# Performance work log

Measured on AMD Instinct MI355X. Metric: run time of the kernel, lower is better.

## Reference

```python
import jax, jax.numpy as jnp
import numpy as np

EMBED = 1024  # embed_dim = hidden_dim = out_dim (n_head=1)
NQ, NK = 4096, 4096
NEG = 1e16


def setup_inputs() -> dict:
    key = jax.random.key(0)
    ks = jax.random.split(key, 10)
    stdv = 1.0 / np.sqrt(EMBED)
    lin = lambda kk: jax.random.uniform(kk, (EMBED, EMBED), jnp.float32, -stdv, stdv)
    vec = lambda kk: jax.random.uniform(kk, (EMBED,), jnp.float32, -stdv, stdv)
    return {
        "q": jax.random.normal(ks[0], (NQ, EMBED), jnp.float32),
        "k": jax.random.normal(ks[1], (NK, EMBED), jnp.float32),
        "mask": jax.random.randint(ks[2], (NQ, NK), 0, 2, jnp.int32),
        "wei": jax.random.uniform(ks[3], (NQ, NK), jnp.float32),
        "Wq": lin(ks[4]), "bq": vec(ks[5]),
        "Wk": lin(ks[6]), "bk": vec(ks[7]),
        "Wp": lin(ks[8]), "bp": vec(ks[9]),
    }


def reference(q, k, mask, wei, Wq, bq, Wk, bk, Wp, bp):
    # Linear projections (torch Linear: x @ W.T + b)
    kx = k @ Wk.T + bk                      # [NK, D]
    qx = q @ Wq.T + bq                      # [NQ, D]
    # dot_product score
    score = qx @ kx.T                       # [NQ, NK]
    bias = (mask.astype(jnp.int32) - 1).astype(score.dtype) * NEG
    score = jax.nn.softmax(score + bias, axis=-1)
    # second weighted+masked softmax pass
    score = jax.nn.softmax(score * wei + bias, axis=-1)
    out = (score @ kx) @ Wp.T + bp          # [NQ, D]
    return out, score
```

## Files before the change

### kernel.cpp

```cpp
#include <hip/hip_runtime.h>


typedef __bf16 bf16;
typedef __bf16 bf16x8 __attribute__((ext_vector_type(8)));
typedef __bf16 bf16x4 __attribute__((ext_vector_type(4)));
typedef float  f32x4  __attribute__((ext_vector_type(4)));
typedef float  f32x16 __attribute__((ext_vector_type(16)));
typedef int    i32x4  __attribute__((ext_vector_type(4)));

typedef __attribute__((address_space(1))) void as1_void;
typedef __attribute__((address_space(3))) void as3_void;

#define NQ  4096
#define NKK 4096
#define EMB 1024

#define BM 128
#define BN 128
#define BK 32

__device__ __forceinline__ void gld_lds16(const void* g, void* l) {
    __builtin_amdgcn_global_load_lds((as1_void*)g, (as3_void*)l, 16, 0, 0);
}

__global__ __launch_bounds__(256) void prep_all(
    const float* __restrict__ q, const float* __restrict__ k,
    const float* __restrict__ Wq, const float* __restrict__ Wk, const float* __restrict__ Wp,
    bf16* __restrict__ qh, bf16* __restrict__ ql,
    bf16* __restrict__ kh, bf16* __restrict__ kl,
    bf16* __restrict__ Wqh, bf16* __restrict__ Wql,
    bf16* __restrict__ Wkh, bf16* __restrict__ Wkl,
    bf16* __restrict__ Wph, bf16* __restrict__ Wpl,
    int nqk, int nw)
{
    const int z = blockIdx.y;
    const float* s; bf16* h; bf16* l; int n;
    switch (z) {
        case 0:  s = q;  h = qh;  l = ql;  n = nqk; break;
        case 1:  s = k;  h = kh;  l = kl;  n = nqk; break;
        case 2:  s = Wq; h = Wqh; l = Wql; n = nw;  break;
        case 3:  s = Wk; h = Wkh; l = Wkl; n = nw;  break;
        default: s = Wp; h = Wph; l = Wpl; n = nw;  break;
    }
    const int i = (blockIdx.x * 256 + threadIdx.x) * 4;
    if (i >= n) return;
    f32x4 v = *(const f32x4*)(s + i);
    bf16x4 hv, lv;
#pragma unroll
    for (int c = 0; c < 4; c++) {
        float x = v[c];
        bf16 hh = (bf16)x;
        hv[c] = hh;
        lv[c] = (bf16)(x - (float)hh);
    }
    *(bf16x4*)(h + i) = hv;
    *(bf16x4*)(l + i) = lv;
}

template<int NS, int MODE>
__global__ __launch_bounds__(256) void reduce_k(
    const float* __restrict__ P, const float* __restrict__ bias,
    float* __restrict__ of, bf16* __restrict__ oh, int n, int Nld)
{
    const int i = (blockIdx.x * 256 + threadIdx.x) * 4;
    if (i >= n) return;
    f32x4 v = *(const f32x4*)(P + i);
#pragma unroll
    for (int s = 1; s < NS; s++)
        v += *(const f32x4*)(P + (size_t)s * n + i);
    if (MODE == 1)
        v += *(const f32x4*)(bias + (i & (Nld - 1)));
    if (MODE == 0) {
        bf16x4 o;
#pragma unroll
        for (int c = 0; c < 4; c++) o[c] = (bf16)v[c];
        *(bf16x4*)(oh + i) = o;
    } else {
        *(f32x4*)(of + i) = v;
    }
}

template<int NSPLIT, int HAS_BIAS, int OUT_BF16>
__global__ __launch_bounds__(256) void gemm_bt(
    const bf16* __restrict__ A, const bf16* __restrict__ B,
    const float* __restrict__ bias,
    float* __restrict__ Cf, bf16* __restrict__ Cb,
    int M, int N, int Ksub, int lda, int ldb)
{
    __shared__ bf16 sA[BM * BK];
    __shared__ bf16 sB[BN * BK];
    const int t    = threadIdx.x;
    const int wave = t >> 6;
    const int lane = t & 63;
    const int l31  = lane & 31;
    const int lhi  = lane >> 5;
    const int wm   = wave >> 1;
    const int wn   = wave & 1;
    const int bm   = blockIdx.y * BM;
    const int bn   = blockIdx.x * BN;
    const int srow = t >> 2;
    const int gseg = (t & 3) ^ ((srow >> 1) & 3);
    const int rsw  = (l31 >> 1) & 3;
    const int kz   = (NSPLIT > 0) ? (int)blockIdx.z : 0;

    A += (size_t)kz * Ksub;
    B += (size_t)kz * Ksub;
    if (NSPLIT > 0) Cf += (size_t)kz * M * N;

    const bf16* ga = A + (size_t)(bm + srow) * lda + gseg * 8;
    const bf16* gb = B + (size_t)(bn + srow) * ldb + gseg * 8;
    char* lA = (char*)sA + wave * 1024;
    char* lB = (char*)sB + wave * 1024;

    f32x16 acc[2][2] = {};

    for (int k0 = 0; k0 < Ksub; k0 += BK) {
        __syncthreads();
        gld_lds16(ga + k0,                      lA);
        gld_lds16(ga + (size_t)64 * lda + k0,   lA + 4096);
        gld_lds16(gb + k0,                      lB);
        gld_lds16(gb + (size_t)64 * ldb + k0,   lB + 4096);
        __syncthreads();
        bf16x8 af[2][2], bfr[2][2];
#pragma unroll
        for (int mi = 0; mi < 2; mi++)
#pragma unroll
            for (int kh = 0; kh < 2; kh++)
                af[mi][kh] = *(const bf16x8*)
                    &sA[(wm * 64 + mi * 32 + l31) * BK + ((kh * 2 + lhi) ^ rsw) * 8];
#pragma unroll
        for (int nj = 0; nj < 2; nj++)
#pragma unroll
            for (int kh = 0; kh < 2; kh++)
                bfr[nj][kh] = *(const bf16x8*)
                    &sB[(wn * 64 + nj * 32 + l31) * BK + ((kh * 2 + lhi) ^ rsw) * 8];
#pragma unroll
        for (int kh = 0; kh < 2; kh++)
#pragma unroll
            for (int mi = 0; mi < 2; mi++)
#pragma unroll
                for (int nj = 0; nj < 2; nj++)
                    acc[mi][nj] = __builtin_amdgcn_mfma_f32_32x32x16_bf16(
                        af[mi][kh], bfr[nj][kh], acc[mi][nj], 0, 0, 0);
    }

#pragma unroll
    for (int mi = 0; mi < 2; mi++)
#pragma unroll
        for (int nj = 0; nj < 2; nj++) {
            const int cg = bn + wn * 64 + nj * 32 + l31;
            const float bv = HAS_BIAS ? bias[cg] : 0.0f;
#pragma unroll
            for (int r = 0; r < 16; r++) {
                const int rg = bm + wm * 64 + mi * 32 + (r & 3) + 8 * (r >> 2) + 4 * lhi;
                const float v = acc[mi][nj][r] + bv;
                const size_t idx = (size_t)rg * N + cg;
                if (NSPLIT > 0)    Cf[idx] = v;
                else if (OUT_BF16) Cb[idx] = (bf16)v;
                else               Cf[idx] = v;
            }
        }
}

template<int BATCH, int HAS_BIAS, int HILO>
__global__ __launch_bounds__(256) void gemm_bt_split(
    const bf16* __restrict__ Ah0, const bf16* __restrict__ Al0,
    const bf16* __restrict__ Bh0, const bf16* __restrict__ Bl0,
    const float* __restrict__ bias0, bf16* __restrict__ Ch0, bf16* __restrict__ Cl0,
    const bf16* __restrict__ Ah1, const bf16* __restrict__ Al1,
    const bf16* __restrict__ Bh1, const bf16* __restrict__ Bl1,
    const float* __restrict__ bias1, bf16* __restrict__ Ch1, bf16* __restrict__ Cl1,
    float* __restrict__ Cf,
    int M, int N, int K)
{
    __shared__ bf16 sAh[BM * BK], sAl[BM * BK], sBh[BN * BK], sBl[BN * BK];
    const int t    = threadIdx.x;
    const int wave = t >> 6;
    const int lane = t & 63;
    const int l31  = lane & 31;
    const int lhi  = lane >> 5;
    const int wm   = wave >> 1;
    const int wn   = wave & 1;
    const int bm   = blockIdx.y * BM;
    const int bn   = blockIdx.x * BN;
    const int srow = t >> 2;
    const int gseg = (t & 3) ^ ((srow >> 1) & 3);
    const int rsw  = (l31 >> 1) & 3;

    const int mt = BATCH ? (int)blockIdx.z : 0;

    const bf16* Ah = (BATCH && mt) ? Ah1 : Ah0;
    const bf16* Al = (BATCH && mt) ? Al1 : Al0;
    const bf16* Bh = (BATCH && mt) ? Bh1 : Bh0;
    const bf16* Bl = (BATCH && mt) ? Bl1 : Bl0;
    const float* bias = (BATCH && mt) ? bias1 : bias0;
    bf16* Ch = (BATCH && mt) ? Ch1 : Ch0;
    bf16* Cl = (BATCH && mt) ? Cl1 : Cl0;

    const size_t offA = (size_t)(bm + srow) * K + gseg * 8;
    const size_t offB = (size_t)(bn + srow) * K + gseg * 8;
    char* lAh = (char*)sAh + wave * 1024;
    char* lAl = (char*)sAl + wave * 1024;
    char* lBh = (char*)sBh + wave * 1024;
    char* lBl = (char*)sBl + wave * 1024;

    f32x16 acc[2][2] = {};

    for (int k0 = 0; k0 < K; k0 += BK) {
        __syncthreads();
        gld_lds16(Ah + offA + k0,                  lAh);
        gld_lds16(Ah + offA + (size_t)64 * K + k0, lAh + 4096);
        gld_lds16(Al + offA + k0,                  lAl);
        gld_lds16(Al + offA + (size_t)64 * K + k0, lAl + 4096);
        gld_lds16(Bh + offB + k0,                  lBh);
        gld_lds16(Bh + offB + (size_t)64 * K + k0, lBh + 4096);
        gld_lds16(Bl + offB + k0,                  lBl);
        gld_lds16(Bl + offB + (size_t)64 * K + k0, lBl + 4096);
        __syncthreads();
#pragma unroll
        for (int kh = 0; kh < 2; kh++) {
            const int ksw = ((kh * 2 + lhi) ^ rsw) * 8;
            bf16x8 ah[2], al[2], bh2[2], bl2[2];
#pragma unroll
            for (int mi = 0; mi < 2; mi++) {
                const int ro = (wm * 64 + mi * 32 + l31) * BK + ksw;
                ah[mi] = *(const bf16x8*)&sAh[ro];
                al[mi] = *(const bf16x8*)&sAl[ro];
            }
#pragma unroll
            for (int nj = 0; nj < 2; nj++) {
                const int ro = (wn * 64 + nj * 32 + l31) * BK + ksw;
                bh2[nj] = *(const bf16x8*)&sBh[ro];
                bl2[nj] = *(const bf16x8*)&sBl[ro];
            }
#pragma unroll
            for (int mi = 0; mi < 2; mi++)
#pragma unroll
                for (int nj = 0; nj < 2; nj++) {
                    acc[mi][nj] = __builtin_amdgcn_mfma_f32_32x32x16_bf16(al[mi], bh2[nj], acc[mi][nj], 0, 0, 0);
                    acc[mi][nj] = __builtin_amdgcn_mfma_f32_32x32x16_bf16(ah[mi], bl2[nj], acc[mi][nj], 0, 0, 0);
                    acc[mi][nj] = __builtin_amdgcn_mfma_f32_32x32x16_bf16(ah[mi], bh2[nj], acc[mi][nj], 0, 0, 0);
                }
        }
    }

#pragma unroll
    for (int mi = 0; mi < 2; mi++)
#pragma unroll
        for (int nj = 0; nj < 2; nj++) {
            const int cg = bn + wn * 64 + nj * 32 + l31;
            const float bv = HAS_BIAS ? bias[cg] : 0.0f;
#pragma unroll
            for (int r = 0; r < 16; r++) {
                const int rg = bm + wm * 64 + mi * 32 + (r & 3) + 8 * (r >> 2) + 4 * lhi;
                const float v = acc[mi][nj][r] + bv;
                const size_t idx = (size_t)rg * N + cg;
                if (HILO) {
                    const bf16 hh = (bf16)v;
                    Ch[idx] = hh;
                    Cl[idx] = (bf16)(v - (float)hh);
                } else {
                    Cf[idx] = v;
                }
            }
        }
}

__global__ __launch_bounds__(256, 2) void gemm_score_kxp(
    const bf16* __restrict__ Ah, const bf16* __restrict__ Al,
    const bf16* __restrict__ Bh, const bf16* __restrict__ Bl,
    float* __restrict__ Cf,
    const bf16* __restrict__ Wp, const bf16* __restrict__ Kx,
    bf16* __restrict__ kxpT)
{
    __shared__ bf16 smem[24576];
    const int t    = threadIdx.x;
    const int wave = t >> 6;
    const int lane = t & 63;
    const int l31  = lane & 31;
    const int lhi  = lane >> 5;
    const int srow = t >> 2;
    const int gseg = (t & 3) ^ ((srow >> 1) & 3);
    const int rsw  = (l31 >> 1) & 3;
    const int bid  = blockIdx.x;

    if (bid < 512) {
        bf16* sAh = smem;
        bf16* sAl = smem + 4096;
        bf16* sBh = smem + 8192;
        bf16* sBl = smem + 16384;
        const int bm = (bid >> 4) * 128;
        const int bn = (bid & 15) * 256;
        const int K  = EMB, N = NKK;

        const size_t offA = (size_t)(bm + srow) * K + gseg * 8;
        const size_t offB = (size_t)(bn + srow) * K + gseg * 8;
        char* lAh = (char*)sAh + wave * 1024;
        char* lAl = (char*)sAl + wave * 1024;
        char* lBh = (char*)sBh + wave * 1024;
        char* lBl = (char*)sBl + wave * 1024;

        f32x16 acc[4][2] = {};

        for (int k0 = 0; k0 < K; k0 += BK) {
            __syncthreads();
            gld_lds16(Ah + offA + k0,                  lAh);
            gld_lds16(Ah + offA + (size_t)64 * K + k0, lAh + 4096);
            gld_lds16(Al + offA + k0,                  lAl);
            gld_lds16(Al + offA + (size_t)64 * K + k0, lAl + 4096);
#pragma unroll
            for (int rb = 0; rb < 4; rb++) {
                gld_lds16(Bh + offB + (size_t)(64 * rb) * K + k0, lBh + rb * 4096);
                gld_lds16(Bl + offB + (size_t)(64 * rb) * K + k0, lBl + rb * 4096);
            }
            __syncthreads();
#pragma unroll
            for (int kh = 0; kh < 2; kh++) {
                const int ksw = ((kh * 2 + lhi) ^ rsw) * 8;
                bf16x8 a_h[4], a_l[4], b_h[2], b_l[2];
#pragma unroll
                for (int mi = 0; mi < 4; mi++) {
                    const int ro = (mi * 32 + l31) * BK + ksw;
                    a_h[mi] = *(const bf16x8*)&sAh[ro];
                    a_l[mi] = *(const bf16x8*)&sAl[ro];
                }
#pragma unroll
                for (int nj = 0; nj < 2; nj++) {
                    const int ro = (wave * 64 + nj * 32 + l31) * BK + ksw;
                    b_h[nj] = *(const bf16x8*)&sBh[ro];
                    b_l[nj] = *(const bf16x8*)&sBl[ro];
                }
#pragma unroll
                for (int mi = 0; mi < 4; mi++)
#pragma unroll
                    for (int nj = 0; nj < 2; nj++) {
                        acc[mi][nj] = __builtin_amdgcn_mfma_f32_32x32x16_bf16(a_l[mi], b_h[nj], acc[mi][nj], 0, 0, 0);
                        acc[mi][nj] = __builtin_amdgcn_mfma_f32_32x32x16_bf16(a_h[mi], b_l[nj], acc[mi][nj], 0, 0, 0);
                        acc[mi][nj] = __builtin_amdgcn_mfma_f32_32x32x16_bf16(a_h[mi], b_h[nj], acc[mi][nj], 0, 0, 0);
                    }
            }
        }

#pragma unroll
        for (int mi = 0; mi < 4; mi++)
#pragma unroll
            for (int nj = 0; nj < 2; nj++) {
                const int cg = bn + wave * 64 + nj * 32 + l31;
#pragma unroll
                for (int r = 0; r < 16; r++) {
                    const int rg = bm + mi * 32 + (r & 3) + 8 * (r >> 2) + 4 * lhi;
                    Cf[(size_t)rg * N + cg] = acc[mi][nj][r];
                }
            }
    } else {
        bf16* sA = smem;
        bf16* sB = smem + 4096;
        const int id = bid - 512;
        const int bn = (id & 31) * 128;
        const int bm = (id >> 5) * 128;
        const int K  = EMB, N = NKK;
        const int wm = wave >> 1;
        const int wn = wave & 1;

        const bf16* ga = Wp + (size_t)(bm + srow) * K + gseg * 8;
        const bf16* gb = Kx + (size_t)(bn + srow) * K + gseg * 8;
        char* lA = (char*)sA + wave * 1024;
        char* lB = (char*)sB + wave * 1024;

        f32x16 acc[2][2] = {};

        for (int k0 = 0; k0 < K; k0 += BK) {
            __syncthreads();
            gld_lds16(ga + k0,                    lA);
            gld_lds16(ga + (size_t)64 * K + k0,   lA + 4096);
            gld_lds16(gb + k0,                    lB);
            gld_lds16(gb + (size_t)64 * K + k0,   lB + 4096);
            __syncthreads();
            bf16x8 af[2][2], bfr[2][2];
#pragma unroll
            for (int mi = 0; mi < 2; mi++)
#pragma unroll
                for (int kh = 0; kh < 2; kh++)
                    af[mi][kh] = *(const bf16x8*)
                        &sA[(wm * 64 + mi * 32 + l31) * BK + ((kh * 2 + lhi) ^ rsw) * 8];
#pragma unroll
            for (int nj = 0; nj < 2; nj++)
#pragma unroll
                for (int kh = 0; kh < 2; kh++)
                    bfr[nj][kh] = *(const bf16x8*)
                        &sB[(wn * 64 + nj * 32 + l31) * BK + ((kh * 2 + lhi) ^ rsw) * 8];
#pragma unroll
            for (int kh = 0; kh < 2; kh++)
#pragma unroll
                for (int mi = 0; mi < 2; mi++)
#pragma unroll
                    for (int nj = 0; nj < 2; nj++)
                        acc[mi][nj] = __builtin_amdgcn_mfma_f32_32x32x16_bf16(
                            af[mi][kh], bfr[nj][kh], acc[mi][nj], 0, 0, 0);
        }

#pragma unroll
        for (int mi = 0; mi < 2; mi++)
#pragma unroll
            for (int nj = 0; nj < 2; nj++) {
                const int cg = bn + wn * 64 + nj * 32 + l31;
#pragma unroll
                for (int r = 0; r < 16; r++) {
                    const int rg = bm + wm * 64 + mi * 32 + (r & 3) + 8 * (r >> 2) + 4 * lhi;
                    kxpT[(size_t)rg * N + cg] = (bf16)acc[mi][nj][r];
                }
            }
    }
}

__device__ __forceinline__ float wred_max(float v) {
#pragma unroll
    for (int off = 32; off > 0; off >>= 1) v = fmaxf(v, __shfl_xor(v, off));
    return v;
}
__device__ __forceinline__ float wred_sum(float v) {
#pragma unroll
    for (int off = 32; off > 0; off >>= 1) v += __shfl_xor(v, off);
    return v;
}

__global__ __launch_bounds__(256) void softmax2_kernel(
    float* __restrict__ score, const int* __restrict__ mask,
    const float* __restrict__ wei, bf16* __restrict__ scoreb)
{
    __shared__ float sred[4];
    const int row = blockIdx.x;
    const int t   = threadIdx.x;
    const size_t base = (size_t)row * NKK + (size_t)t * 16;
    const int wv = t >> 6, ln = t & 63;

    float l[16], w[16];
    unsigned mb = 0;
#pragma unroll
    for (int c = 0; c < 4; c++) {
        *(f32x4*)(l + 4 * c) = *(const f32x4*)(score + base + 4 * c);
        *(f32x4*)(w + 4 * c) = *(const f32x4*)(wei + base + 4 * c);
        i32x4 mv = *(const i32x4*)(mask + base + 4 * c);
#pragma unroll
        for (int j = 0; j < 4; j++) if (mv[j] != 0) mb |= 1u << (4 * c + j);
    }

    float mx = -__builtin_inff();
#pragma unroll
    for (int s = 0; s < 16; s++) if (mb & (1u << s)) mx = fmaxf(mx, l[s]);
    mx = wred_max(mx);
    if (ln == 0) sred[wv] = mx;
    __syncthreads();
    mx = fmaxf(fmaxf(sred[0], sred[1]), fmaxf(sred[2], sred[3]));
    __syncthreads();
    float sum = 0.f;
#pragma unroll
    for (int s = 0; s < 16; s++) {
        const float e = (mb & (1u << s)) ? __expf(l[s] - mx) : 0.f;
        l[s] = e; sum += e;
    }
    sum = wred_sum(sum);
    if (ln == 0) sred[wv] = sum;
    __syncthreads();
    sum = sred[0] + sred[1] + sred[2] + sred[3];
    __syncthreads();
    const float inv1 = 1.0f / sum;

#pragma unroll
    for (int s = 0; s < 16; s++) l[s] = l[s] * inv1 * w[s];

    float mx2 = -__builtin_inff();
#pragma unroll
    for (int s = 0; s < 16; s++) if (mb & (1u << s)) mx2 = fmaxf(mx2, l[s]);
    mx2 = wred_max(mx2);
    if (ln == 0) sred[wv] = mx2;
    __syncthreads();
    mx2 = fmaxf(fmaxf(sred[0], sred[1]), fmaxf(sred[2], sred[3]));
    __syncthreads();
    float sum2 = 0.f;
#pragma unroll
    for (int s = 0; s < 16; s++) {
        const float e = (mb & (1u << s)) ? __expf(l[s] - mx2) : 0.f;
        l[s] = e; sum2 += e;
    }
    sum2 = wred_sum(sum2);
    if (ln == 0) sred[wv] = sum2;
    __syncthreads();
    sum2 = sred[0] + sred[1] + sred[2] + sred[3];
    const float inv2 = 1.0f / sum2;

#pragma unroll
    for (int c = 0; c < 4; c++) {
        f32x4 pv;
#pragma unroll
        for (int j = 0; j < 4; j++) pv[j] = l[4 * c + j] * inv2;
        __builtin_nontemporal_store(pv, (f32x4*)(score + base + 4 * c));
#pragma unroll
        for (int j = 0; j < 4; j++) l[4 * c + j] = pv[j];
    }
    bf16x8 b0, b1;
#pragma unroll
    for (int j = 0; j < 8; j++) { b0[j] = (bf16)l[j]; b1[j] = (bf16)l[8 + j]; }
    *(bf16x8*)(scoreb + base)     = b0;
    *(bf16x8*)(scoreb + base + 8) = b1;
}

extern "C" void kernel_launch(void* const* d_in, const int* in_sizes, int n_in,
                              void* d_out, int out_size, void* d_ws, size_t ws_size,
                              hipStream_t stream)
{
    (void)in_sizes; (void)n_in; (void)out_size;
    const float* q    = (const float*)d_in[0];
    const float* k    = (const float*)d_in[1];
    const int*   mask = (const int*)  d_in[2];
    const float* wei  = (const float*)d_in[3];
    const float* Wq   = (const float*)d_in[4];
    const float* bq   = (const float*)d_in[5];
    const float* Wk   = (const float*)d_in[6];
    const float* bk   = (const float*)d_in[7];
    const float* Wp   = (const float*)d_in[8];
    const float* bp   = (const float*)d_in[9];

    float* out   = (float*)d_out;
    float* score = (float*)d_out + (size_t)NQ * EMB;

    char* ws = (char*)d_ws;
    size_t off = 0;
    auto alloc = [&](size_t bytes) -> char* {
        char* p = ws + off; off += (bytes + 255) & ~(size_t)255; return p;
    };
    const size_t n_qk = (size_t)NQ * EMB;
    const size_t n_w  = (size_t)EMB * EMB;
    const size_t n_sc = (size_t)NQ * NKK;

    bf16* qh   = (bf16*)alloc(n_qk * 2);
    bf16* ql   = (bf16*)alloc(n_qk * 2);
    bf16* kh   = (bf16*)alloc(n_qk * 2);
    bf16* kl   = (bf16*)alloc(n_qk * 2);
    bf16* qxh  = (bf16*)alloc(n_qk * 2);
    bf16* qxl  = (bf16*)alloc(n_qk * 2);
    bf16* kxh  = (bf16*)alloc(n_qk * 2);
    bf16* kxl  = (bf16*)alloc(n_qk * 2);
    bf16* Wqh  = (bf16*)alloc(n_w * 2);
    bf16* Wql  = (bf16*)alloc(n_w * 2);
    bf16* Wkh  = (bf16*)alloc(n_w * 2);
    bf16* Wkl  = (bf16*)alloc(n_w * 2);
    bf16* Wpb  = (bf16*)alloc(n_w * 2);
    bf16* Wpl  = (bf16*)alloc(n_w * 2);
    bf16* kxpTb = (bf16*)alloc(n_qk * 2);
    bf16* scoreb = (bf16*)alloc(n_sc * 2);
    const size_t base_off = off;
    float* P = (float*)alloc(2 * n_qk * 4);
    const bool ws_ok = (off <= ws_size);
    if (base_off > ws_size) return;

    const int MN = (int)n_qk;

    prep_all<<<dim3(n_qk / 1024, 5), 256, 0, stream>>>(
        q, k, Wq, Wk, Wp,
        qh, ql, kh, kl, Wqh, Wql, Wkh, Wkl, Wpb, Wpl,
        (int)n_qk, (int)n_w);

    gemm_bt_split<1, 1, 1><<<dim3(EMB / BN, NQ / BM, 2), 256, 0, stream>>>(
        qh, ql, Wqh, Wql, bq, qxh, qxl,
        kh, kl, Wkh, Wkl, bk, kxh, kxl,
        nullptr, NQ, EMB, EMB);

    gemm_score_kxp<<<dim3(768), 256, 0, stream>>>(
        qxh, qxl, kxh, kxl, score, Wpb, kxh, kxpTb);

    softmax2_kernel<<<dim3(NQ), 256, 0, stream>>>(score, mask, wei, scoreb);

    if (ws_ok) {
        gemm_bt<2, 0, 0><<<dim3(EMB / BN, NQ / BM, 2), 256, 0, stream>>>(
            scoreb, kxpTb, nullptr, P, nullptr, NQ, EMB, NKK / 2, NKK, NKK);
        reduce_k<2, 1><<<dim3(MN / 1024), 256, 0, stream>>>(
            P, bp, out, nullptr, MN, EMB);
    } else {
        gemm_bt<0, 1, 0><<<dim3(EMB / BN, NQ / BM), 256, 0, stream>>>(
            scoreb, kxpTb, bp, out, nullptr, NQ, EMB, NKK, NKK, NKK);
    }
}
```

Baseline: 483.7 us.

## Rewrite score GEMM as 256x256 double-buffered tile with fused kxp tail

Replaces the 768-block score/kxp kernel with 256 blocks of 512 threads, each computing a 256x256 score tile using double-buffered LDS staging, interleaved prefetch, and raised MFMA priority. Each block then computes one 128x128 tile of the Wp·Kx product serially after its score tile instead of in separate blocks. This aims to increase operand reuse and overlap loads with MFMA, but it uses 128KB of LDS per block, which limits occupancy. Serialising the kxp work onto the same blocks also lengthens each block's critical path.

```diff
diff --git a/kernel.cpp b/kernel.cpp
--- a/kernel.cpp
+++ b/kernel.cpp
@@ -266,150 +266,163 @@
         }
 }
 
-__global__ __launch_bounds__(256, 2) void gemm_score_kxp(
+__global__ __launch_bounds__(512, 2) void gemm_score256(
     const bf16* __restrict__ Ah, const bf16* __restrict__ Al,
     const bf16* __restrict__ Bh, const bf16* __restrict__ Bl,
     float* __restrict__ Cf,
     const bf16* __restrict__ Wp, const bf16* __restrict__ Kx,
     bf16* __restrict__ kxpT)
 {
-    __shared__ bf16 smem[24576];
+    __shared__ bf16 smem[65536];
     const int t    = threadIdx.x;
     const int wave = t >> 6;
     const int lane = t & 63;
     const int l31  = lane & 31;
     const int lhi  = lane >> 5;
+    const int wm   = wave >> 2;
+    const int wn   = wave & 3;
+    const int bm   = (blockIdx.x >> 4) * 256;
+    const int bn   = (blockIdx.x & 15) * 256;
     const int srow = t >> 2;
     const int gseg = (t & 3) ^ ((srow >> 1) & 3);
     const int rsw  = (l31 >> 1) & 3;
-    const int bid  = blockIdx.x;
-
-    if (bid < 512) {
-        bf16* sAh = smem;
-        bf16* sAl = smem + 4096;
-        bf16* sBh = smem + 8192;
-        bf16* sBl = smem + 16384;
-        const int bm = (bid >> 4) * 128;
-        const int bn = (bid & 15) * 256;
-        const int K  = EMB, N = NKK;
-
-        const size_t offA = (size_t)(bm + srow) * K + gseg * 8;
-        const size_t offB = (size_t)(bn + srow) * K + gseg * 8;
-        char* lAh = (char*)sAh + wave * 1024;
-        char* lAl = (char*)sAl + wave * 1024;
-        char* lBh = (char*)sBh + wave * 1024;
-        char* lBl = (char*)sBl + wave * 1024;
-
-        f32x16 acc[4][2] = {};
-
-        for (int k0 = 0; k0 < K; k0 += BK) {
-            __syncthreads();
-            gld_lds16(Ah + offA + k0,                  lAh);
-            gld_lds16(Ah + offA + (size_t)64 * K + k0, lAh + 4096);
-            gld_lds16(Al + offA + k0,                  lAl);
-            gld_lds16(Al + offA + (size_t)64 * K + k0, lAl + 4096);
-#pragma unroll
-            for (int rb = 0; rb < 4; rb++) {
-                gld_lds16(Bh + offB + (size_t)(64 * rb) * K + k0, lBh + rb * 4096);
-                gld_lds16(Bl + offB + (size_t)(64 * rb) * K + k0, lBl + rb * 4096);
-            }
-            __syncthreads();
+    const int K    = EMB;
+    const int NT   = K / BK;
+
+    const bf16* gAh = Ah + (size_t)(bm + srow) * K + gseg * 8;
+    const bf16* gAl = Al + (size_t)(bm + srow) * K + gseg * 8;
+    const bf16* gBh = Bh + (size_t)(bn + srow) * K + gseg * 8;
+    const bf16* gBl = Bl + (size_t)(bn + srow) * K + gseg * 8;
+
+    auto stageA = [&](int buf, int k0) {
+        char* L = (char*)smem + buf * 65536 + wave * 1024;
+        gld_lds16(gAh + k0,                   L + 0);
+        gld_lds16(gAh + (size_t)128 * K + k0, L + 8192);
+        gld_lds16(gAl + k0,                   L + 16384);
+        gld_lds16(gAl + (size_t)128 * K + k0, L + 16384 + 8192);
+    };
+    auto stageB = [&](int buf, int k0) {
+        char* L = (char*)smem + buf * 65536 + wave * 1024;
+        gld_lds16(gBh + k0,                   L + 32768);
+        gld_lds16(gBh + (size_t)128 * K + k0, L + 32768 + 8192);
+        gld_lds16(gBl + k0,                   L + 49152);
+        gld_lds16(gBl + (size_t)128 * K + k0, L + 49152 + 8192);
+    };
+
+    f32x16 acc[4][2] = {};
+
+    stageA(0, 0);
+    stageB(0, 0);
+    asm volatile("s_waitcnt vmcnt(0)" ::: "memory");
+    __builtin_amdgcn_s_barrier();
+
+    for (int tt = 0; tt < NT; ++tt) {
+        const int cur = tt & 1;
+        const int cb  = cur * 32768;
+        const int kn  = (tt + 1) * BK;
+        bf16x8 bh2[2], bl2[2];
+#pragma unroll
+        for (int ph = 0; ph < 4; ++ph) {
+            const int kh   = ph >> 1;
+            const int half = ph & 1;
+            const int ksw  = ((kh * 2 + lhi) ^ rsw) * 8;
+            if (half == 0) {
+#pragma unroll
+                for (int nj = 0; nj < 2; nj++) {
+                    const int ro = cb + 16384 + (wn * 64 + nj * 32 + l31) * BK + ksw;
+                    bh2[nj] = *(const bf16x8*)&smem[ro];
+                    bl2[nj] = *(const bf16x8*)&smem[ro + 8192];
+                }
+            }
+            bf16x8 a_h[2], a_l[2];
+#pragma unroll
+            for (int i = 0; i < 2; i++) {
+                const int ro = cb + (wm * 128 + (half * 2 + i) * 32 + l31) * BK + ksw;
+                a_h[i] = *(const bf16x8*)&smem[ro];
+                a_l[i] = *(const bf16x8*)&smem[ro + 8192];
+            }
+            if (tt < NT - 1) {
+                if (ph == 0)      stageA(cur ^ 1, kn);
+                else if (ph == 1) stageB(cur ^ 1, kn);
+            }
+            __builtin_amdgcn_s_barrier();
+            asm volatile("s_waitcnt lgkmcnt(0)" ::: "memory");
+            __builtin_amdgcn_sched_barrier(0);
+            __builtin_amdgcn_s_setprio(1);
+#pragma unroll
+            for (int i = 0; i < 2; i++) {
+                const int mi = half * 2 + i;
+#pragma unroll
+                for (int nj = 0; nj < 2; nj++) {
+                    acc[mi][nj] = __builtin_amdgcn_mfma_f32_32x32x16_bf16(a_l[i], bh2[nj], acc[mi][nj], 0, 0, 0);
+                    acc[mi][nj] = __builtin_amdgcn_mfma_f32_32x32x16_bf16(a_h[i], bl2[nj], acc[mi][nj], 0, 0, 0);
+                    acc[mi][nj] = __builtin_amdgcn_mfma_f32_32x32x16_bf16(a_h[i], bh2[nj], acc[mi][nj], 0, 0, 0);
+                }
+            }
+            __builtin_amdgcn_s_setprio(0);
+            if (ph == 3)
+                asm volatile("s_waitcnt vmcnt(0)" ::: "memory");
+            __builtin_amdgcn_s_barrier();
+        }
+    }
+
+#pragma unroll
+    for (int mi = 0; mi < 4; mi++)
+#pragma unroll
+        for (int nj = 0; nj < 2; nj++) {
+            const int cg = bn + wn * 64 + nj * 32 + l31;
+#pragma unroll
+            for (int r = 0; r < 16; r++) {
+                const int rg = bm + wm * 128 + mi * 32 + (r & 3) + 8 * (r >> 2) + 4 * lhi;
+                Cf[(size_t)rg * NKK + cg] = acc[mi][nj][r];
+            }
+        }
+
+    {
+        const int km  = (blockIdx.x >> 5) * 128;
+        const int kn2 = (blockIdx.x & 31) * 128;
+        const int wm4 = wave >> 1;
+        const int wn2 = wave & 1;
+        const bf16* gW = Wp + (size_t)(km  + srow) * K + gseg * 8;
+        const bf16* gX = Kx + (size_t)(kn2 + srow) * K + gseg * 8;
+        auto stageK = [&](int buf, int k0) {
+            char* L = (char*)smem + buf * 16384 + wave * 1024;
+            gld_lds16(gW + k0, L);
+            gld_lds16(gX + k0, L + 8192);
+        };
+        f32x16 ac2[2] = {};
+        stageK(0, 0);
+        for (int it = 0; it < NT; ++it) {
+            const int cur = it & 1;
+            const int cb  = cur * 8192;
+            if (it < NT - 1) {
+                stageK(cur ^ 1, (it + 1) * BK);
+                asm volatile("s_waitcnt vmcnt(2)" ::: "memory");
+            } else {
+                asm volatile("s_waitcnt vmcnt(0)" ::: "memory");
+            }
+            __builtin_amdgcn_s_barrier();
 #pragma unroll
             for (int kh = 0; kh < 2; kh++) {
                 const int ksw = ((kh * 2 + lhi) ^ rsw) * 8;
-                bf16x8 a_h[4], a_l[4], b_h[2], b_l[2];
-#pragma unroll
-                for (int mi = 0; mi < 4; mi++) {
-                    const int ro = (mi * 32 + l31) * BK + ksw;
-                    a_h[mi] = *(const bf16x8*)&sAh[ro];
-                    a_l[mi] = *(const bf16x8*)&sAl[ro];
-                }
-#pragma unroll
-                for (int nj = 0; nj < 2; nj++) {
-                    const int ro = (wave * 64 + nj * 32 + l31) * BK + ksw;
-                    b_h[nj] = *(const bf16x8*)&sBh[ro];
-                    b_l[nj] = *(const bf16x8*)&sBl[ro];
-                }
-#pragma unroll
-                for (int mi = 0; mi < 4; mi++)
-#pragma unroll
-                    for (int nj = 0; nj < 2; nj++) {
-                        acc[mi][nj] = __builtin_amdgcn_mfma_f32_32x32x16_bf16(a_l[mi], b_h[nj], acc[mi][nj], 0, 0, 0);
-                        acc[mi][nj] = __builtin_amdgcn_mfma_f32_32x32x16_bf16(a_h[mi], b_l[nj], acc[mi][nj], 0, 0, 0);
-                        acc[mi][nj] = __builtin_amdgcn_mfma_f32_32x32x16_bf16(a_h[mi], b_h[nj], acc[mi][nj], 0, 0, 0);
-                    }
-            }
-        }
-
-#pragma unroll
-        for (int mi = 0; mi < 4; mi++)
-#pragma unroll
-            for (int nj = 0; nj < 2; nj++) {
-                const int cg = bn + wave * 64 + nj * 32 + l31;
-#pragma unroll
-                for (int r = 0; r < 16; r++) {
-                    const int rg = bm + mi * 32 + (r & 3) + 8 * (r >> 2) + 4 * lhi;
-                    Cf[(size_t)rg * N + cg] = acc[mi][nj][r];
-                }
-            }
-    } else {
-        bf16* sA = smem;
-        bf16* sB = smem + 4096;
-        const int id = bid - 512;
-        const int bn = (id & 31) * 128;
-        const int bm = (id >> 5) * 128;
-        const int K  = EMB, N = NKK;
-        const int wm = wave >> 1;
-        const int wn = wave & 1;
-
-        const bf16* ga = Wp + (size_t)(bm + srow) * K + gseg * 8;
-        const bf16* gb = Kx + (size_t)(bn + srow) * K + gseg * 8;
-        char* lA = (char*)sA + wave * 1024;
-        char* lB = (char*)sB + wave * 1024;
-
-        f32x16 acc[2][2] = {};
-
-        for (int k0 = 0; k0 < K; k0 += BK) {
-            __syncthreads();
-            gld_lds16(ga + k0,                    lA);
-            gld_lds16(ga + (size_t)64 * K + k0,   lA + 4096);
-            gld_lds16(gb + k0,                    lB);
-            gld_lds16(gb + (size_t)64 * K + k0,   lB + 4096);
-            __syncthreads();
-            bf16x8 af[2][2], bfr[2][2];
-#pragma unroll
-            for (int mi = 0; mi < 2; mi++)
-#pragma unroll
-                for (int kh = 0; kh < 2; kh++)
-                    af[mi][kh] = *(const bf16x8*)
-                        &sA[(wm * 64 + mi * 32 + l31) * BK + ((kh * 2 + lhi) ^ rsw) * 8];
-#pragma unroll
-            for (int nj = 0; nj < 2; nj++)
-#pragma unroll
-                for (int kh = 0; kh < 2; kh++)
-                    bfr[nj][kh] = *(const bf16x8*)
-                        &sB[(wn * 64 + nj * 32 + l31) * BK + ((kh * 2 + lhi) ^ rsw) * 8];
-#pragma unroll
-            for (int kh = 0; kh < 2; kh++)
-#pragma unroll
-                for (int mi = 0; mi < 2; mi++)
-#pragma unroll
-                    for (int nj = 0; nj < 2; nj++)
-                        acc[mi][nj] = __builtin_amdgcn_mfma_f32_32x32x16_bf16(
-                            af[mi][kh], bfr[nj][kh], acc[mi][nj], 0, 0, 0);
-        }
-
-#pragma unroll
-        for (int mi = 0; mi < 2; mi++)
-#pragma unroll
-            for (int nj = 0; nj < 2; nj++) {
-                const int cg = bn + wn * 64 + nj * 32 + l31;
-#pragma unroll
-                for (int r = 0; r < 16; r++) {
-                    const int rg = bm + wm * 64 + mi * 32 + (r & 3) + 8 * (r >> 2) + 4 * lhi;
-                    kxpT[(size_t)rg * N + cg] = (bf16)acc[mi][nj][r];
-                }
-            }
+                bf16x8 av  = *(const bf16x8*)&smem[cb + (wm4 * 32 + l31) * BK + ksw];
+                bf16x8 bv0 = *(const bf16x8*)&smem[cb + 4096 + (wn2 * 64 + l31) * BK + ksw];
+                bf16x8 bv1 = *(const bf16x8*)&smem[cb + 4096 + (wn2 * 64 + 32 + l31) * BK + ksw];
+                ac2[0] = __builtin_amdgcn_mfma_f32_32x32x16_bf16(av, bv0, ac2[0], 0, 0, 0);
+                ac2[1] = __builtin_amdgcn_mfma_f32_32x32x16_bf16(av, bv1, ac2[1], 0, 0, 0);
+            }
+            asm volatile("s_waitcnt lgkmcnt(0)" ::: "memory");
+            __builtin_amdgcn_s_barrier();
+        }
+#pragma unroll
+        for (int nj = 0; nj < 2; nj++) {
+            const int cg = kn2 + wn2 * 64 + nj * 32 + l31;
+#pragma unroll
+            for (int r = 0; r < 16; r++) {
+                const int rg = km + wm4 * 32 + (r & 3) + 8 * (r >> 2) + 4 * lhi;
+                kxpT[(size_t)rg * NKK + cg] = (bf16)ac2[nj][r];
+            }
+        }
     }
 }
 
@@ -566,7 +579,7 @@
         kh, kl, Wkh, Wkl, bk, kxh, kxl,
         nullptr, NQ, EMB, EMB);
 
-    gemm_score_kxp<<<dim3(768), 256, 0, stream>>>(
+    gemm_score256<<<dim3(256), 512, 0, stream>>>(
         qxh, qxl, kxh, kxl, score, Wpb, kxh, kxpTb);
 
     softmax2_kernel<<<dim3(NQ), 256, 0, stream>>>(score, mask, wei, scoreb);
```

Result: no change. 476.3 us (-1.5%).
